# Performance work log

Measured on AMD Instinct MI355X. Metric: run time of the kernel, lower is better.

Reference implementation:

```python
import jax, jax.numpy as jnp
import numpy as np

B, LQ, LP, H = 16, 2048, 2048, 1024

def setup_inputs() -> dict:
    key = jax.random.key(0)
    kq, kp, kw = jax.random.split(key, 3)
    q = jax.random.normal(kq, (B, LQ, H), dtype=jnp.float32)
    p = jax.random.normal(kp, (B, LP, H), dtype=jnp.float32)
    W = jax.random.normal(kw, (H, H), dtype=jnp.float32) * (1.0 / np.sqrt(H))
    b = jnp.zeros((H,), dtype=jnp.float32)
    return {"q": q, "p": p, "W": W, "b": b}

def reference(q, p, W, b):
    # shared linear + ReLU projections (torch Linear: x @ W.T + b)
    q_lin = jax.nn.relu(jnp.einsum('bqh,oh->bqo', q, W) + b)  # [B,LQ,H]
    p_lin = jax.nn.relu(jnp.einsum('bph,oh->bpo', p, W) + b)  # [B,LP,H]
    # unscaled cross-attention scores: p_lin @ q_lin^T -> [B,LP,LQ]
    scores = jnp.einsum('bpd,bqd->bpq', p_lin, q_lin)
    att = jax.nn.softmax(scores, axis=2)
    # context-aware query: att @ q_lin -> [B,LP,H]
    return jnp.einsum('bpq,bqd->bpd', att, q_lin)
```

## Files before the change

kernel.cpp:

```cpp
#include <hip/hip_runtime.h>


#define LQN 2048
#define LPN 2048
#define HD  1024
#define NBATCH 16

typedef _Float16 half8 __attribute__((ext_vector_type(8)));
typedef _Float16 half4_t __attribute__((ext_vector_type(4)));
typedef float f32x4 __attribute__((ext_vector_type(4)));

#define GLP(src, dst) __builtin_amdgcn_global_load_lds(                          \
    (const __attribute__((address_space(1))) void*)(src),                        \
    (__attribute__((address_space(3))) void*)(dst), 16, 0, 0)

__global__ __launch_bounds__(256) void cvt_f32_f16(const float* __restrict__ in,
                                                   _Float16* __restrict__ out,
                                                   long n4) {
  long i0 = (long)blockIdx.x * blockDim.x + threadIdx.x;
  long stride = (long)gridDim.x * blockDim.x;
  for (long i = i0; i < n4; i += stride) {
    float4 v = ((const float4*)in)[i];
    half4_t h = {(_Float16)v.x, (_Float16)v.y, (_Float16)v.z, (_Float16)v.w};
    ((half4_t*)out)[i] = h;
  }
}

__global__ __launch_bounds__(256) void transpose_k(const _Float16* __restrict__ in,
                                                   _Float16* __restrict__ out) {
  __shared__ _Float16 t[64][72];
  const int bz = blockIdx.z;
  const int q0 = blockIdx.x * 64;
  const int d0 = blockIdx.y * 64;
  const int tt = threadIdx.x;
  const int ql = tt & 63, dg = tt >> 6;
  const _Float16* src = in + ((size_t)bz * LQN + q0 + ql) * HD + d0 + dg * 16;
  half8 v0 = *(const half8*)(src);
  half8 v1 = *(const half8*)(src + 8);
  int g0 = (dg * 2) ^ (ql & 7);
  int g1 = (dg * 2 + 1) ^ (ql & 7);
  *(half8*)&t[ql][g0 * 8] = v0;
  *(half8*)&t[ql][g1 * 8] = v1;
  __syncthreads();
  const int dl = tt & 63, qg = tt >> 6;
  half8 o0, o1;
#pragma unroll
  for (int j = 0; j < 8; ++j) {
    int qq = qg * 16 + j;
    o0[j] = t[qq][(((dl >> 3) ^ (qq & 7)) << 3) + (dl & 7)];
  }
#pragma unroll
  for (int j = 0; j < 8; ++j) {
    int qq = qg * 16 + 8 + j;
    o1[j] = t[qq][(((dl >> 3) ^ (qq & 7)) << 3) + (dl & 7)];
  }
  _Float16* dst = out + ((size_t)bz * HD + d0 + dl) * LQN + q0 + qg * 16;
  *(half8*)dst = o0;
  *(half8*)(dst + 8) = o1;
}


#define SYNC_PRE                                        \
  __builtin_amdgcn_sched_barrier(0);                    \
  __builtin_amdgcn_s_barrier();                         \
  asm volatile("s_waitcnt lgkmcnt(0)" ::: "memory");    \
  __builtin_amdgcn_sched_barrier(0);                    \
  __builtin_amdgcn_s_setprio(1);

#define SYNC_POST                                       \
  __builtin_amdgcn_s_setprio(0);                        \
  __builtin_amdgcn_sched_barrier(0);                    \
  __builtin_amdgcn_s_barrier();

#define SYNC_POST_VM                                    \
  __builtin_amdgcn_s_setprio(0);                        \
  __builtin_amdgcn_sched_barrier(0);                    \
  asm volatile("s_waitcnt vmcnt(4)" ::: "memory");      \
  __builtin_amdgcn_s_barrier();

#define LOADA(qm, buf)                                                            \
  _Pragma("unroll")                                                               \
  for (int mi = 0; mi < 4; ++mi) {                                                \
    areg[mi][0] = *(const half8*)(smA + (buf)*32768 + a0 + ((qm)*4+mi)*4096);     \
    areg[mi][1] = *(const half8*)(smA + (buf)*32768 + a1 + ((qm)*4+mi)*4096);     \
  }

#define LOADB(qn, buf)                                                            \
  _Pragma("unroll")                                                               \
  for (int ni = 0; ni < 2; ++ni) {                                                \
    bregs[qn][ni][0] = *(const half8*)(smB + (buf)*32768 + b0 + ((qn)*2+ni)*8192);\
    bregs[qn][ni][1] = *(const half8*)(smB + (buf)*32768 + b1 + ((qn)*2+ni)*8192);\
  }

#define STAGEA(t, h, buf) do {                                                    \
  GLP(gA + (size_t)((h)*128)*lda + (size_t)(t)*64,                                \
      smW + (buf)*32768 + (h)*16384 + wid*1024);                                  \
  GLP(gA + (size_t)((h)*128+64)*lda + (size_t)(t)*64,                             \
      smW + (buf)*32768 + (h)*16384 + 8192 + wid*1024);                           \
} while (0)

#define STAGEB(t, h, buf) do {                                                    \
  GLP(gB + (size_t)((h)*128)*ldb + (size_t)(t)*64,                                \
      smW + 65536 + (buf)*32768 + (h)*16384 + wid*1024);                          \
  GLP(gB + (size_t)((h)*128+64)*ldb + (size_t)(t)*64,                             \
      smW + 65536 + (buf)*32768 + (h)*16384 + 8192 + wid*1024);                   \
} while (0)

#define DO_MFMA(qm, qn)                                                           \
  _Pragma("unroll")                                                               \
  for (int mi = 0; mi < 4; ++mi) {                                                \
    _Pragma("unroll")                                                             \
    for (int ni = 0; ni < 2; ++ni) {                                              \
      acc[(qm)*4+mi][(qn)*2+ni] = __builtin_amdgcn_mfma_f32_16x16x32_f16(         \
          areg[mi][0], bregs[qn][ni][0], acc[(qm)*4+mi][(qn)*2+ni], 0, 0, 0);     \
      acc[(qm)*4+mi][(qn)*2+ni] = __builtin_amdgcn_mfma_f32_16x16x32_f16(         \
          areg[mi][1], bregs[qn][ni][1], acc[(qm)*4+mi][(qn)*2+ni], 0, 0, 0);     \
    }                                                                             \
  }

template <int EPI>
__global__ __launch_bounds__(512, 2) void gemm8p(
    const _Float16* __restrict__ A, const _Float16* __restrict__ B,
    const float* __restrict__ bias, void* __restrict__ Cv,
    int K, int lda, int ldb, int ldc,
    long sAz, long sBz, long sCz) {
  extern __shared__ __align__(16) char smem[];
  const char* smA = smem;
  const char* smB = smem + 65536;
  char* smW = smem;

  const int tid = threadIdx.x;
  const int lane = tid & 63, wid = tid >> 6;
  const int l16 = lane & 15, lhi = lane >> 4;
  const int wr = wid >> 2, wcn = wid & 3;

  const int mask = (l16 & 7) << 4;
  const int a0 = (wr * 2048 + l16 * 128 + lhi * 16) ^ mask;
  const int a1 = a0 ^ 64;
  const int b0 = (wcn * 2048 + l16 * 128 + lhi * 16) ^ mask;
  const int b1 = b0 ^ 64;

  const int srow = tid >> 3;
  const int scol = (((tid & 7) ^ ((tid >> 3) & 7)) << 3);

  const int bm0 = blockIdx.x * 256, bn0 = blockIdx.y * 256;
  const _Float16* gA = A + (size_t)blockIdx.z * sAz + (size_t)(bm0 + srow) * lda + scol;
  const _Float16* gB = B + (size_t)blockIdx.z * sBz + (size_t)(bn0 + srow) * ldb + scol;

  const int NT = K >> 6, NI = K >> 7;

  f32x4 acc[8][4] = {};
  half8 areg[4][2], bregs[2][2][2];

  STAGEA(0, 0, 0); STAGEB(0, 0, 0);
  STAGEA(0, 1, 0); STAGEB(0, 1, 0);
  STAGEA(1, 0, 1); STAGEB(1, 0, 1);
  __builtin_amdgcn_sched_barrier(0);
  asm volatile("s_waitcnt vmcnt(4)" ::: "memory");
  __builtin_amdgcn_s_barrier();

  for (int i = 0; i < NI; ++i) {
    const int t1 = 2 * i + 1;
    int t2 = 2 * i + 2; if (t2 > NT - 1) t2 = NT - 1;
    int t3 = 2 * i + 3; if (t3 > NT - 1) t3 = NT - 1;
    LOADA(0, 0) LOADB(0, 0) STAGEA(t1, 1, 1);
    SYNC_PRE DO_MFMA(0, 0) SYNC_POST
    LOADB(1, 0) STAGEB(t1, 1, 1);
    SYNC_PRE DO_MFMA(0, 1) SYNC_POST
    LOADA(1, 0) STAGEA(t2, 0, 0);
    SYNC_PRE DO_MFMA(1, 0) SYNC_POST
    STAGEB(t2, 0, 0);
    SYNC_PRE DO_MFMA(1, 1) SYNC_POST_VM
    LOADA(0, 1) LOADB(0, 1) STAGEA(t2, 1, 0);
    SYNC_PRE DO_MFMA(0, 0) SYNC_POST
    LOADB(1, 1) STAGEB(t2, 1, 0);
    SYNC_PRE DO_MFMA(0, 1) SYNC_POST
    LOADA(1, 1) STAGEA(t3, 0, 1);
    SYNC_PRE DO_MFMA(1, 0) SYNC_POST
    STAGEB(t3, 0, 1);
    SYNC_PRE DO_MFMA(1, 1) SYNC_POST_VM
  }

  if constexpr (EPI == 0) {
    float* Cb = (float*)Cv + (size_t)blockIdx.z * sCz;
#pragma unroll
    for (int m = 0; m < 8; ++m) {
      int row0 = bm0 + m * 32 + wr * 16 + lhi * 4;
#pragma unroll
      for (int n = 0; n < 4; ++n) {
        int col = bn0 + n * 64 + wcn * 16 + l16;
#pragma unroll
        for (int v = 0; v < 4; ++v)
          Cb[(size_t)(row0 + v) * ldc + col] = acc[m][n][v];
      }
    }
  } else {
    _Float16* Cb = (_Float16*)Cv;
#pragma unroll
    for (int n = 0; n < 4; ++n) {
      int col = bn0 + n * 64 + wcn * 16 + l16;
      float bv = bias[col];
#pragma unroll
      for (int m = 0; m < 8; ++m) {
        int row0 = bm0 + m * 32 + wr * 16 + lhi * 4;
        Cb[(size_t)(row0 + 0) * ldc + col] = (_Float16)fmaxf(acc[m][n][0] + bv, 0.f);
        Cb[(size_t)(row0 + 1) * ldc + col] = (_Float16)fmaxf(acc[m][n][1] + bv, 0.f);
        Cb[(size_t)(row0 + 2) * ldc + col] = (_Float16)fmaxf(acc[m][n][2] + bv, 0.f);
        Cb[(size_t)(row0 + 3) * ldc + col] = (_Float16)fmaxf(acc[m][n][3] + bv, 0.f);
      }
    }
  }
}

__global__ __launch_bounds__(256) void softmax_k(float* __restrict__ buf) {
  __shared__ float red[4];
  const int t = threadIdx.x;
  float* s = buf + (size_t)blockIdx.x * 2048;
  float4 v0 = ((const float4*)s)[t * 2];
  float4 v1 = ((const float4*)s)[t * 2 + 1];
  float m = fmaxf(fmaxf(fmaxf(v0.x, v0.y), fmaxf(v0.z, v0.w)),
                  fmaxf(fmaxf(v1.x, v1.y), fmaxf(v1.z, v1.w)));
#pragma unroll
  for (int o = 32; o; o >>= 1) m = fmaxf(m, __shfl_xor(m, o));
  if ((t & 63) == 0) red[t >> 6] = m;
  __syncthreads();
  m = fmaxf(fmaxf(red[0], red[1]), fmaxf(red[2], red[3]));
  float e[8];
  e[0] = __expf(v0.x - m); e[1] = __expf(v0.y - m);
  e[2] = __expf(v0.z - m); e[3] = __expf(v0.w - m);
  e[4] = __expf(v1.x - m); e[5] = __expf(v1.y - m);
  e[6] = __expf(v1.z - m); e[7] = __expf(v1.w - m);
  float sum = ((e[0] + e[1]) + (e[2] + e[3])) + ((e[4] + e[5]) + (e[6] + e[7]));
#pragma unroll
  for (int o = 32; o; o >>= 1) sum += __shfl_xor(sum, o);
  __syncthreads();
  if ((t & 63) == 0) red[t >> 6] = sum;
  __syncthreads();
  sum = (red[0] + red[1]) + (red[2] + red[3]);
  float inv = 1.f / sum;
  half8 h;
  h[0] = (_Float16)(e[0] * inv); h[1] = (_Float16)(e[1] * inv);
  h[2] = (_Float16)(e[2] * inv); h[3] = (_Float16)(e[3] * inv);
  h[4] = (_Float16)(e[4] * inv); h[5] = (_Float16)(e[5] * inv);
  h[6] = (_Float16)(e[6] * inv); h[7] = (_Float16)(e[7] * inv);
  ((half8*)s)[t] = h;
}

extern "C" void kernel_launch(void* const* d_in, const int* in_sizes, int n_in,
                              void* d_out, int out_size, void* d_ws, size_t ws_size,
                              hipStream_t stream) {
  const float* q = (const float*)d_in[0];
  const float* p = (const float*)d_in[1];
  const float* W = (const float*)d_in[2];
  const float* bias = (const float*)d_in[3];
  float* out = (float*)d_out;
  char* ws = (char*)d_ws;

  _Float16* qf    = (_Float16*)(ws);
  _Float16* pf    = (_Float16*)(ws + 67108864L);
  _Float16* qlin  = (_Float16*)(ws + 134217728L);
  _Float16* plin  = (_Float16*)(ws + 201326592L);
  _Float16* qlinT = (_Float16*)(ws + 268435456L);
  _Float16* Wf    = (_Float16*)(ws + 335544320L);
  float* scores   = (float*)ws;

  const long nQ = (long)NBATCH * LQN * HD;
  const size_t SH = 131072;

  cvt_f32_f16<<<2048, 256, 0, stream>>>(q, qf, nQ / 4);
  cvt_f32_f16<<<2048, 256, 0, stream>>>(p, pf, nQ / 4);
  cvt_f32_f16<<<64, 256, 0, stream>>>(W, Wf, (long)HD * HD / 4);

  gemm8p<1><<<dim3(2 * NBATCH * LQN / 256, HD / 256, 1), 512, SH, stream>>>(
      qf, Wf, bias, qlin, HD, HD, HD, HD, 0, 0, 0);

  transpose_k<<<dim3(LQN / 64, HD / 64, NBATCH), 256, 0, stream>>>(qlin, qlinT);

  for (int c = 0; c < 2; ++c) {
    int bz0 = c * 8;
    gemm8p<0><<<dim3(LPN / 256, LQN / 256, 8), 512, SH, stream>>>(
        plin + (size_t)bz0 * LPN * HD, qlin + (size_t)bz0 * LQN * HD,
        (const float*)0, scores,
        HD, HD, HD, LQN,
        (long)LPN * HD, (long)LQN * HD, (long)LPN * LQN);
    softmax_k<<<8 * LPN, 256, 0, stream>>>(scores);
    gemm8p<0><<<dim3(LPN / 256, HD / 256, 8), 512, SH, stream>>>(
        (const _Float16*)scores, qlinT + (size_t)bz0 * HD * LQN,
        (const float*)0, out + (size_t)bz0 * LPN * HD,
        LQN, 2 * LQN, LQN, HD,
        (long)LPN * 2 * LQN, (long)HD * LQN, (long)LPN * HD);
  }
}
```

Measured before the change: 598.4 us.

## Fuse tile-local softmax into score GEMM epilogue and add block-swizzled tile mapping

The score GEMM epilogue now computes a per-tile row max and exp-sum, writes unnormalised fp16 probabilities directly, and records (max, sum) side data per 256-column tile. A light renorm kernel then rescales each row to the global softmax. This replaces the fp32 score write, the separate softmax read/write pass and the strided fp16 layout. It also remaps block indices with a stride-8 interleave so that different blocks share A/B tiles in cache. The cost is an extra fp16 read-modify-write pass plus epilogue shuffles and LDS reductions.

```diff
diff --git a/kernel.cpp b/kernel.cpp
--- a/kernel.cpp
+++ b/kernel.cpp
@@ -122,7 +122,7 @@
 __global__ __launch_bounds__(512, 2) void gemm8p(
     const _Float16* __restrict__ A, const _Float16* __restrict__ B,
     const float* __restrict__ bias, void* __restrict__ Cv,
-    int K, int lda, int ldb, int ldc,
+    float2* __restrict__ side, int K, int lda, int ldb, int ldc,
     long sAz, long sBz, long sCz) {
   extern __shared__ __align__(16) char smem[];
   const char* smA = smem;
@@ -134,6 +134,14 @@
   const int l16 = lane & 15, lhi = lane >> 4;
   const int wr = wid >> 2, wcn = wid & 3;
 
+  const int nx = gridDim.x;
+  const int d = blockIdx.y * nx + blockIdx.x;
+  const int cpx = (nx * gridDim.y) >> 3;
+  const int t_ = (d & 7) * cpx + (d >> 3);
+  const int xsh = 31 - __builtin_clz(nx);
+  const int bn0 = (t_ & (nx - 1)) << 8;
+  const int bm0 = (t_ >> xsh) << 8;
+
   const int mask = (l16 & 7) << 4;
   const int a0 = (wr * 2048 + l16 * 128 + lhi * 16) ^ mask;
   const int a1 = a0 ^ 64;
@@ -143,7 +151,6 @@
   const int srow = tid >> 3;
   const int scol = (((tid & 7) ^ ((tid >> 3) & 7)) << 3);
 
-  const int bm0 = blockIdx.x * 256, bn0 = blockIdx.y * 256;
   const _Float16* gA = A + (size_t)blockIdx.z * sAz + (size_t)(bm0 + srow) * lda + scol;
   const _Float16* gB = B + (size_t)blockIdx.z * sBz + (size_t)(bn0 + srow) * ldb + scol;
 
@@ -194,7 +201,7 @@
           Cb[(size_t)(row0 + v) * ldc + col] = acc[m][n][v];
       }
     }
-  } else {
+  } else if constexpr (EPI == 1) {
     _Float16* Cb = (_Float16*)Cv;
 #pragma unroll
     for (int n = 0; n < 4; ++n) {
@@ -209,41 +216,123 @@
         Cb[(size_t)(row0 + 3) * ldc + col] = (_Float16)fmaxf(acc[m][n][3] + bv, 0.f);
       }
     }
-  }
-}
-
-__global__ __launch_bounds__(256) void softmax_k(float* __restrict__ buf) {
-  __shared__ float red[4];
-  const int t = threadIdx.x;
-  float* s = buf + (size_t)blockIdx.x * 2048;
-  float4 v0 = ((const float4*)s)[t * 2];
-  float4 v1 = ((const float4*)s)[t * 2 + 1];
-  float m = fmaxf(fmaxf(fmaxf(v0.x, v0.y), fmaxf(v0.z, v0.w)),
-                  fmaxf(fmaxf(v1.x, v1.y), fmaxf(v1.z, v1.w)));
-#pragma unroll
-  for (int o = 32; o; o >>= 1) m = fmaxf(m, __shfl_xor(m, o));
-  if ((t & 63) == 0) red[t >> 6] = m;
-  __syncthreads();
-  m = fmaxf(fmaxf(red[0], red[1]), fmaxf(red[2], red[3]));
-  float e[8];
-  e[0] = __expf(v0.x - m); e[1] = __expf(v0.y - m);
-  e[2] = __expf(v0.z - m); e[3] = __expf(v0.w - m);
-  e[4] = __expf(v1.x - m); e[5] = __expf(v1.y - m);
-  e[6] = __expf(v1.z - m); e[7] = __expf(v1.w - m);
-  float sum = ((e[0] + e[1]) + (e[2] + e[3])) + ((e[4] + e[5]) + (e[6] + e[7]));
-#pragma unroll
-  for (int o = 32; o; o >>= 1) sum += __shfl_xor(sum, o);
-  __syncthreads();
-  if ((t & 63) == 0) red[t >> 6] = sum;
-  __syncthreads();
-  sum = (red[0] + red[1]) + (red[2] + red[3]);
-  float inv = 1.f / sum;
-  half8 h;
-  h[0] = (_Float16)(e[0] * inv); h[1] = (_Float16)(e[1] * inv);
-  h[2] = (_Float16)(e[2] * inv); h[3] = (_Float16)(e[3] * inv);
-  h[4] = (_Float16)(e[4] * inv); h[5] = (_Float16)(e[5] * inv);
-  h[6] = (_Float16)(e[6] * inv); h[7] = (_Float16)(e[7] * inv);
-  ((half8*)s)[t] = h;
+  } else {
+    float* redm = (float*)smW;
+    float* reds = (float*)(smW + 4096);
+    float tm[8][4];
+#pragma unroll
+    for (int m = 0; m < 8; ++m)
+#pragma unroll
+      for (int v = 0; v < 4; ++v)
+        tm[m][v] = fmaxf(fmaxf(acc[m][0][v], acc[m][1][v]),
+                         fmaxf(acc[m][2][v], acc[m][3][v]));
+#pragma unroll
+    for (int o = 1; o < 16; o <<= 1)
+#pragma unroll
+      for (int m = 0; m < 8; ++m)
+#pragma unroll
+        for (int v = 0; v < 4; ++v)
+          tm[m][v] = fmaxf(tm[m][v], __shfl_xor(tm[m][v], o));
+    if (l16 == 0) {
+#pragma unroll
+      for (int m = 0; m < 8; ++m)
+#pragma unroll
+        for (int v = 0; v < 4; ++v)
+          redm[(m * 32 + wr * 16 + lhi * 4 + v) * 4 + wcn] = tm[m][v];
+    }
+    __syncthreads();
+    float rm[8][4], rs[8][4];
+#pragma unroll
+    for (int m = 0; m < 8; ++m)
+#pragma unroll
+      for (int v = 0; v < 4; ++v) {
+        float4 q4 = ((const float4*)redm)[m * 32 + wr * 16 + lhi * 4 + v];
+        rm[m][v] = fmaxf(fmaxf(q4.x, q4.y), fmaxf(q4.z, q4.w));
+      }
+#pragma unroll
+    for (int m = 0; m < 8; ++m)
+#pragma unroll
+      for (int v = 0; v < 4; ++v) {
+        float s = 0.f;
+#pragma unroll
+        for (int n = 0; n < 4; ++n) {
+          float e = __expf(acc[m][n][v] - rm[m][v]);
+          acc[m][n][v] = e;
+          s += e;
+        }
+        tm[m][v] = s;
+      }
+#pragma unroll
+    for (int o = 1; o < 16; o <<= 1)
+#pragma unroll
+      for (int m = 0; m < 8; ++m)
+#pragma unroll
+        for (int v = 0; v < 4; ++v)
+          tm[m][v] += __shfl_xor(tm[m][v], o);
+    __syncthreads();
+    if (l16 == 0) {
+#pragma unroll
+      for (int m = 0; m < 8; ++m)
+#pragma unroll
+        for (int v = 0; v < 4; ++v)
+          reds[(m * 32 + wr * 16 + lhi * 4 + v) * 4 + wcn] = tm[m][v];
+    }
+    __syncthreads();
+#pragma unroll
+    for (int m = 0; m < 8; ++m)
+#pragma unroll
+      for (int v = 0; v < 4; ++v) {
+        float4 q4 = ((const float4*)reds)[m * 32 + wr * 16 + lhi * 4 + v];
+        rs[m][v] = (q4.x + q4.y) + (q4.z + q4.w);
+      }
+    _Float16* Cb = (_Float16*)Cv + (size_t)blockIdx.z * sCz;
+#pragma unroll
+    for (int n = 0; n < 4; ++n) {
+      int col = bn0 + n * 64 + wcn * 16 + l16;
+#pragma unroll
+      for (int m = 0; m < 8; ++m) {
+        int row0 = bm0 + m * 32 + wr * 16 + lhi * 4;
+        Cb[(size_t)(row0 + 0) * ldc + col] = (_Float16)acc[m][n][0];
+        Cb[(size_t)(row0 + 1) * ldc + col] = (_Float16)acc[m][n][1];
+        Cb[(size_t)(row0 + 2) * ldc + col] = (_Float16)acc[m][n][2];
+        Cb[(size_t)(row0 + 3) * ldc + col] = (_Float16)acc[m][n][3];
+      }
+    }
+    if (l16 == 0 && wcn == 0) {
+      float2* sb = side + ((size_t)blockIdx.z * 2048 + bm0) * 8 + (bn0 >> 8);
+#pragma unroll
+      for (int m = 0; m < 8; ++m)
+#pragma unroll
+        for (int v = 0; v < 4; ++v) {
+          int r = m * 32 + wr * 16 + lhi * 4 + v;
+          sb[(size_t)r * 8] = make_float2(rm[m][v], rs[m][v]);
+        }
+    }
+  }
+}
+
+__global__ __launch_bounds__(256) void renorm_k(_Float16* __restrict__ P,
+                                                const float2* __restrict__ side) {
+  const int row = blockIdx.x;
+  const int bz = blockIdx.y;
+  const float2* sd = side + ((size_t)bz * 2048 + row) * 8;
+  float mt[8], st[8];
+#pragma unroll
+  for (int t = 0; t < 8; ++t) { float2 v = sd[t]; mt[t] = v.x; st[t] = v.y; }
+  float m = mt[0];
+#pragma unroll
+  for (int t = 1; t < 8; ++t) m = fmaxf(m, mt[t]);
+  float S = 0.f;
+#pragma unroll
+  for (int t = 0; t < 8; ++t) S += st[t] * __expf(mt[t] - m);
+  const float inv = 1.f / S;
+  const int tid = threadIdx.x;
+  const float sc = __expf(mt[tid >> 5] - m) * inv;
+  _Float16* p = P + (((size_t)bz * 2048 + row) * 2048) + tid * 8;
+  half8 v = *(half8*)p;
+#pragma unroll
+  for (int j = 0; j < 8; ++j) v[j] = (_Float16)((float)v[j] * sc);
+  *(half8*)p = v;
 }
 
 extern "C" void kernel_launch(void* const* d_in, const int* in_sizes, int n_in,
@@ -262,7 +351,8 @@
   _Float16* plin  = (_Float16*)(ws + 201326592L);
   _Float16* qlinT = (_Float16*)(ws + 268435456L);
   _Float16* Wf    = (_Float16*)(ws + 335544320L);
-  float* scores   = (float*)ws;
+  _Float16* Pbuf  = (_Float16*)(ws);
+  float2*   side  = (float2*)(ws + 67108864L);
 
   const long nQ = (long)NBATCH * LQN * HD;
   const size_t SH = 131072;
@@ -271,23 +361,23 @@
   cvt_f32_f16<<<2048, 256, 0, stream>>>(p, pf, nQ / 4);
   cvt_f32_f16<<<64, 256, 0, stream>>>(W, Wf, (long)HD * HD / 4);
 
-  gemm8p<1><<<dim3(2 * NBATCH * LQN / 256, HD / 256, 1), 512, SH, stream>>>(
-      qf, Wf, bias, qlin, HD, HD, HD, HD, 0, 0, 0);
+  gemm8p<1><<<dim3(HD / 256, 2 * NBATCH * LQN / 256, 1), 512, SH, stream>>>(
+      qf, Wf, bias, qlin, (float2*)0, HD, HD, HD, HD, 0, 0, 0);
 
   transpose_k<<<dim3(LQN / 64, HD / 64, NBATCH), 256, 0, stream>>>(qlin, qlinT);
 
   for (int c = 0; c < 2; ++c) {
     int bz0 = c * 8;
-    gemm8p<0><<<dim3(LPN / 256, LQN / 256, 8), 512, SH, stream>>>(
+    gemm8p<2><<<dim3(LQN / 256, LPN / 256, 8), 512, SH, stream>>>(
         plin + (size_t)bz0 * LPN * HD, qlin + (size_t)bz0 * LQN * HD,
-        (const float*)0, scores,
+        (const float*)0, Pbuf, side,
         HD, HD, HD, LQN,
         (long)LPN * HD, (long)LQN * HD, (long)LPN * LQN);
-    softmax_k<<<8 * LPN, 256, 0, stream>>>(scores);
-    gemm8p<0><<<dim3(LPN / 256, HD / 256, 8), 512, SH, stream>>>(
-        (const _Float16*)scores, qlinT + (size_t)bz0 * HD * LQN,
-        (const float*)0, out + (size_t)bz0 * LPN * HD,
-        LQN, 2 * LQN, LQN, HD,
-        (long)LPN * 2 * LQN, (long)HD * LQN, (long)LPN * HD);
-  }
-}
+    renorm_k<<<dim3(LPN, 8), 256, 0, stream>>>(Pbuf, side);
+    gemm8p<0><<<dim3(HD / 256, LPN / 256, 8), 512, SH, stream>>>(
+        Pbuf, qlinT + (size_t)bz0 * HD * LQN,
+        (const float*)0, out + (size_t)bz0 * LPN * HD, (float2*)0,
+        LQN, LQN, LQN, HD,
+        (long)LPN * LQN, (long)HD * LQN, (long)LPN * HD);
+  }
+}
```

Measured after the change: 590.3 us. About the same (-1.4%).
